# Optimization experiments

Measured on AMD Instinct MI355X. Metric: run time of the kernel, lower is better.

The kernel has to match this reference:

```python
import jax, jax.numpy as jnp
import numpy as np

B, N, D, H, SEEDS = 32, 2048, 256, 8, 32
DH = D // H
SCALE = 1.0 / np.sqrt(D)  # 1/sqrt(dim_V), as in MAB


def setup_inputs() -> dict:
    key = jax.random.key(0)
    ks = jax.random.split(key, 7)
    w_std = 1.0 / np.sqrt(D)  # ~ xavier scale for (D, D)
    x = jax.random.normal(ks[0], (B, N, D), dtype=jnp.float32)
    lengths = jax.random.randint(ks[1], (B,), 1, N + 1).astype(jnp.int64)
    S = jax.random.normal(ks[2], (1, SEEDS, D), dtype=jnp.float32) * w_std
    Wq = jax.random.normal(ks[3], (D, D), dtype=jnp.float32) * w_std
    Wk = jax.random.normal(ks[4], (D, D), dtype=jnp.float32) * w_std
    Wv = jax.random.normal(ks[5], (D, D), dtype=jnp.float32) * w_std
    Wo = jax.random.normal(ks[6], (D, D), dtype=jnp.float32) * w_std
    return {"x": x, "lengths": lengths, "S": S, "Wq": Wq, "Wk": Wk, "Wv": Wv, "Wo": Wo}


def reference(x, lengths, S, Wq, Wk, Wv, Wo):
    # PMA with norm=None: seeds attend over the (length-masked) input set.
    b, n, d = x.shape
    seeds = S.shape[1]
    # Linear projections (torch Linear: y = x @ W.T, bias=False)
    Q = jnp.einsum("bsd,ed->bse", jnp.broadcast_to(S, (b, seeds, d)), Wq)  # (B,SEEDS,D)
    K = jnp.einsum("bnd,ed->bne", x, Wk)  # (B,N,D)
    V = jnp.einsum("bnd,ed->bne", x, Wv)
    # mask=['K'] -> zero K,V rows beyond lengths
    col_mask = (jnp.arange(n)[None, :] < lengths[:, None]).astype(x.dtype)  # (B,N)
    K = K * col_mask[:, :, None]
    V = V * col_mask[:, :, None]
    # head split: (h b) s d  <=>  b h s d
    Qh = Q.reshape(b, seeds, H, DH).transpose(0, 2, 1, 3)  # (B,H,SEEDS,DH)
    Kh = K.reshape(b, n, H, DH).transpose(0, 2, 1, 3)      # (B,H,N,DH)
    Vh = V.reshape(b, n, H, DH).transpose(0, 2, 1, 3)
    scores = jnp.einsum("bhsd,bhnd->bhsn", Qh, Kh) * SCALE  # (B,H,SEEDS,N)
    exp = jnp.exp(scores)
    # set_softmax: two-sided length masks, normalize over keys with +1e-15
    row_mask = (jnp.arange(seeds)[None, :] < lengths[:, None]).astype(x.dtype)  # (B,SEEDS)
    exp = exp * row_mask[:, None, :, None] * col_mask[:, None, None, :]
    A = exp / (exp.sum(axis=3, keepdims=True) + 1e-15)
    Oh = Qh + jnp.einsum("bhsn,bhnd->bhsd", A, Vh)  # residual on Q_
    O = Oh.transpose(0, 2, 1, 3).reshape(b, seeds, d)  # merge heads
    # norm0/norm1 are None (norm=None in PMA)
    O = O + jax.nn.relu(jnp.einsum("bse,de->bsd", O, Wo))
    O = O * row_mask[:, :, None]  # final apply_masks(O, lengths)
    lengths_out = jnp.minimum(jnp.full_like(lengths, seeds), lengths)
    return O, lengths_out
```

## Files before the change

kernel.cpp:

```cpp
#include <hip/hip_runtime.h>
#include <hip/hip_bf16.h>
#include <cstdint>

#define BATCH 32
#define NKEY 2048
#define DIM 256
#define NHEAD 8
#define SEEDS 32
#define DHEAD 32
#define SCALE 0.0625f
#define NCHUNK 16
#define KCH 128
#define KT 32
#define PART_BYTES 17408

typedef unsigned short u16;
typedef __attribute__((ext_vector_type(8))) short s16x8;
typedef __attribute__((ext_vector_type(8))) unsigned short u16x8;
typedef __attribute__((ext_vector_type(4))) unsigned short u16x4;
typedef __attribute__((ext_vector_type(4))) float f32x4;

__device__ __forceinline__ u16 f2bf(float f) {
    unsigned u = __float_as_uint(f);
    u += 0x7FFFu + ((u >> 16) & 1u);
    return (u16)(u >> 16);
}
__device__ __forceinline__ float bf2f(u16 h) {
    return __uint_as_float(((unsigned)h) << 16);
}
__device__ __forceinline__ int get_len(const int* lens, int b) {
    return (lens[1] == 0) ? lens[2 * b] : lens[b];
}
__device__ __forceinline__ u16x8 cvt8(const float* p) {
    f32x4 a = *(const f32x4*)p;
    f32x4 b = *(const f32x4*)(p + 4);
    u16x8 r;
    r[0] = f2bf(a[0]); r[1] = f2bf(a[1]); r[2] = f2bf(a[2]); r[3] = f2bf(a[3]);
    r[4] = f2bf(b[0]); r[5] = f2bf(b[1]); r[6] = f2bf(b[2]); r[7] = f2bf(b[3]);
    return r;
}
__device__ __forceinline__ void glds16(const u16* g, u16* l) {
    __builtin_amdgcn_global_load_lds(
        (const __attribute__((address_space(1))) unsigned int*)g,
        (__attribute__((address_space(3))) unsigned int*)l, 16, 0, 0);
}

#define XGROUPS 2097152
#define WGROUPS 16384
__global__ __launch_bounds__(256) void cvt_kernel(const float* __restrict__ x,
                                                  const float* __restrict__ Wk,
                                                  const float* __restrict__ Wv,
                                                  u16* __restrict__ xb,
                                                  u16* __restrict__ wb) {
    size_t g = (size_t)blockIdx.x * 256 + threadIdx.x;
    size_t stride = (size_t)gridDim.x * 256;
    for (; g < XGROUPS + WGROUPS; g += stride) {
        const float* src;
        u16* dst;
        if (g < XGROUPS) {
            src = x + g * 8;
            dst = xb + g * 8;
        } else {
            size_t gw = g - XGROUPS;
            dst = wb + gw * 8;
            src = (gw < 8192) ? (Wk + gw * 8) : (Wv + (gw - 8192) * 8);
        }
        *(u16x8*)dst = cvt8(src);
    }
}

__global__ __launch_bounds__(256) void qproj_kernel(const float* __restrict__ S,
                                                    const float* __restrict__ Wq,
                                                    float* __restrict__ qf) {
    int s = blockIdx.x;
    int e = threadIdx.x;
    __shared__ float srow[DIM];
    srow[e] = S[s * DIM + e];
    __syncthreads();
    const float* wr = Wq + (size_t)e * DIM;
    float acc = 0.f;
#pragma unroll 4
    for (int d = 0; d < DIM; d += 4) {
        f32x4 w = *(const f32x4*)(wr + d);
        acc += srow[d] * w[0] + srow[d + 1] * w[1] + srow[d + 2] * w[2] + srow[d + 3] * w[3];
    }
    qf[s * DIM + e] = acc;
}

#define BM 128
#define BN 128
#define BK 32

__global__ __launch_bounds__(256) void kv_gemm_kernel(const u16* __restrict__ xb,
                                                      const u16* __restrict__ wb,
                                                      u16* __restrict__ kg,
                                                      u16* __restrict__ vt) {
    __shared__ u16 Alds[BM * BK];
    __shared__ u16 Blds[BM * BK];
    int bid = blockIdx.x;
    int swz = (bid & 7) * 256 + (bid >> 3);
    int nb = swz & 3;
    int mb = swz >> 2;
    const u16* asrc = xb + (size_t)mb * BM * DIM;
    const u16* bsrc = wb + (size_t)nb * BN * DIM;

    int tid = threadIdx.x;
    int lane = tid & 63;
    int wid = tid >> 6;
    int wr = wid >> 1, wc = wid & 1;
    int k8 = (lane >> 4) * 8;
    int fr = lane & 15;

    int srow = wid * 32 + (lane >> 2);
    int scol = (lane & 3) * 8;

    f32x4 acc[4][4];
#pragma unroll
    for (int m = 0; m < 4; m++)
#pragma unroll
        for (int n = 0; n < 4; n++) acc[m][n] = (f32x4){0.f, 0.f, 0.f, 0.f};

    for (int k0 = 0; k0 < DIM; k0 += BK) {
        const u16* ga = asrc + (size_t)srow * DIM + k0 + scol;
        const u16* gb = bsrc + (size_t)srow * DIM + k0 + scol;
        glds16(ga,            &Alds[(wid * 32) * BK]);
        glds16(ga + 16 * DIM, &Alds[(wid * 32 + 16) * BK]);
        glds16(gb,            &Blds[(wid * 32) * BK]);
        glds16(gb + 16 * DIM, &Blds[(wid * 32 + 16) * BK]);
        __syncthreads();

        s16x8 af[4], bfg[4];
#pragma unroll
        for (int m = 0; m < 4; m++)
            af[m] = *(const s16x8*)&Alds[(wr * 64 + m * 16 + fr) * BK + k8];
#pragma unroll
        for (int n = 0; n < 4; n++)
            bfg[n] = *(const s16x8*)&Blds[(wc * 64 + n * 16 + fr) * BK + k8];
#pragma unroll
        for (int m = 0; m < 4; m++)
#pragma unroll
            for (int n = 0; n < 4; n++)
                acc[m][n] = __builtin_amdgcn_mfma_f32_16x16x32_bf16(af[m], bfg[n], acc[m][n], 0, 0, 0);
        __syncthreads();
    }

    int gmbase = mb * BM + wr * 64 + (lane >> 4) * 4;
    int gnbase = nb * BN + wc * 64 + fr;
#pragma unroll
    for (int m = 0; m < 4; m++) {
        int r0 = gmbase + m * 16;
#pragma unroll
        for (int n = 0; n < 4; n++) {
            int gc = gnbase + n * 16;
            if (gc < 256) {
#pragma unroll
                for (int q = 0; q < 4; q++) {
                    int r = r0 + q;
                    kg[(size_t)r * 256 + (gc ^ ((r & 7) << 3))] = f2bf(acc[m][n][q]);
                }
            } else {
                int dh = gc - 256;
                int bidx = r0 >> 11, key = r0 & 2047;
                u16x4 v = {f2bf(acc[m][n][0]), f2bf(acc[m][n][1]),
                           f2bf(acc[m][n][2]), f2bf(acc[m][n][3])};
                *(u16x4*)&vt[((size_t)bidx * 256 + dh) * NKEY + key] = v;
            }
        }
    }
}

__global__ __launch_bounds__(512) void attn_kernel(const u16* __restrict__ kg,
                                                   const u16* __restrict__ vt,
                                                   const float* __restrict__ qf,
                                                   const int* __restrict__ lens,
                                                   char* __restrict__ partials) {
    int b = blockIdx.y, chunk = blockIdx.x;
    int len = get_len(lens, b);
    int n0 = chunk * KCH;
    int n1 = min(n0 + KCH, len);
    int tid = threadIdx.x;
    int lane = tid & 63;
    int h = tid >> 6;
    int fr = lane & 15;
    int g = lane >> 4;
    int k8 = g * 8;

    __shared__ u16 Klds[KT * 256];
    __shared__ u16 VTlds[256 * KT];
    __shared__ u16 Plds[NHEAD][32][32];

    s16x8 qb[2];
    qb[0] = (s16x8)cvt8(qf + (size_t)(fr) * DIM + h * DHEAD + k8);
    qb[1] = (s16x8)cvt8(qf + (size_t)(16 + fr) * DIM + h * DHEAD + k8);

    f32x4 accp[2][2];
#pragma unroll
    for (int i = 0; i < 2; i++)
#pragma unroll
        for (int j = 0; j < 2; j++) accp[i][j] = (f32x4){0.f, 0.f, 0.f, 0.f};
    float dsum[2] = {0.f, 0.f};

    int nk = n1 - n0;
    int nsteps = (nk > 0) ? ((nk + KT - 1) / KT) : 0;

    for (int t = 0; t < nsteps; t++) {
        {
            const u16* gk = kg + ((size_t)(b * NKEY + n0 + t * KT + h * 4) + (lane >> 5)) * 256
                               + (lane & 31) * 8;
            glds16(gk,           &Klds[(h * 4) * 256]);
            glds16(gk + 2 * 256, &Klds[(h * 4 + 2) * 256]);
            const u16* gv = vt + ((size_t)b * 256 + h * 32 + (lane >> 2)) * NKEY
                               + (n0 + t * KT) + (lane & 3) * 8;
            glds16(gv,            &VTlds[(h * 32) * KT]);
            glds16(gv + 16 * NKEY, &VTlds[(h * 32 + 16) * KT]);
        }
        __syncthreads();

        int rem = nk - t * KT;

        s16x8 ka[2];
#pragma unroll
        for (int m = 0; m < 2; m++)
            ka[m] = *(const s16x8*)&Klds[(m * 16 + fr) * 256 + (((h * 4 + g) ^ (fr & 7)) << 3)];
        f32x4 sc[2][2];
#pragma unroll
        for (int m = 0; m < 2; m++)
#pragma unroll
            for (int n = 0; n < 2; n++) {
                f32x4 z = (f32x4){0.f, 0.f, 0.f, 0.f};
                sc[m][n] = __builtin_amdgcn_mfma_f32_16x16x32_bf16(ka[m], qb[n], z, 0, 0, 0);
            }

#pragma unroll
        for (int m = 0; m < 2; m++) {
            int kbase = m * 16 + g * 4;
            int col = (((kbase >> 3) ^ (fr & 3)) << 3) + (kbase & 7);
#pragma unroll
            for (int n = 0; n < 2; n++) {
                u16x4 pv;
#pragma unroll
                for (int q = 0; q < 4; q++) {
                    float e = (kbase + q < rem) ? __expf(sc[m][n][q] * SCALE) : 0.f;
                    dsum[n] += e;
                    pv[q] = f2bf(e);
                }
                *(u16x4*)&Plds[h][n * 16 + fr][col] = pv;
            }
        }

        s16x8 pa[2], vb[2];
        int rcol = (g ^ (fr & 3)) << 3;
#pragma unroll
        for (int m = 0; m < 2; m++)
            pa[m] = *(const s16x8*)&Plds[h][m * 16 + fr][rcol];
#pragma unroll
        for (int n = 0; n < 2; n++)
            vb[n] = *(const s16x8*)&VTlds[(h * 32 + n * 16 + fr) * KT + k8];
#pragma unroll
        for (int m = 0; m < 2; m++)
#pragma unroll
            for (int n = 0; n < 2; n++)
                accp[m][n] = __builtin_amdgcn_mfma_f32_16x16x32_bf16(pa[m], vb[n], accp[m][n], 0, 0, 0);
        __syncthreads();
    }

    dsum[0] += __shfl_xor(dsum[0], 16);
    dsum[0] += __shfl_xor(dsum[0], 32);
    dsum[1] += __shfl_xor(dsum[1], 16);
    dsum[1] += __shfl_xor(dsum[1], 32);

    char* pb = partials + ((size_t)b * NCHUNK + chunk) * PART_BYTES;
    u16* pnum = (u16*)pb;
    float* pden = (float*)(pb + 16384);
#pragma unroll
    for (int m = 0; m < 2; m++)
#pragma unroll
        for (int n = 0; n < 2; n++)
#pragma unroll
            for (int q = 0; q < 4; q++)
                pnum[(size_t)(m * 16 + g * 4 + q) * DIM + h * DHEAD + n * 16 + fr] =
                    f2bf(accp[m][n][q]);
    if (lane < 16) {
        pden[h * 32 + fr] = dsum[0];
        pden[h * 32 + 16 + fr] = dsum[1];
    }
}

__global__ __launch_bounds__(256) void reduce_kernel(const char* __restrict__ partials,
                                                     const float* __restrict__ qf,
                                                     const int* __restrict__ lens,
                                                     float* __restrict__ opre,
                                                     float* __restrict__ outlen) {
    int b = blockIdx.x;
    int p = threadIdx.x;
    int h = p >> 5, s = p & 31;
    float denom = 0.f;
    float num[DHEAD];
#pragma unroll
    for (int j = 0; j < DHEAD; j++) num[j] = 0.f;
    for (int c = 0; c < NCHUNK; c++) {
        const char* pb = partials + ((size_t)b * NCHUNK + c) * PART_BYTES;
        denom += ((const float*)(pb + 16384))[p];
        const u16* pn = (const u16*)pb;
#pragma unroll
        for (int j = 0; j < DHEAD; j += 8) {
            u16x8 u = *(const u16x8*)&pn[(size_t)s * DIM + h * DHEAD + j];
#pragma unroll
            for (int t = 0; t < 8; t++) num[j + t] += bf2f(u[t]);
        }
    }
    float inv = 1.f / (denom + 1e-15f);
    size_t obase = ((size_t)b * SEEDS + s) * DIM + h * DHEAD;
#pragma unroll
    for (int j = 0; j < DHEAD; j++) {
        opre[obase + j] = qf[s * DIM + h * DHEAD + j] + num[j] * inv;
    }
    if (p == 0) outlen[b] = (float)min(SEEDS, get_len(lens, b));
}

__global__ __launch_bounds__(256) void epilogue_kernel(const float* __restrict__ opre,
                                                       const float* __restrict__ Wo,
                                                       const int* __restrict__ lens,
                                                       float* __restrict__ out) {
    int s = blockIdx.x, b = blockIdx.y;
    int d = threadIdx.x;
    size_t rbase = ((size_t)b * SEEDS + s) * DIM;
    if (s >= get_len(lens, b)) {
        out[rbase + d] = 0.f;
        return;
    }
    __shared__ float orow[DIM];
    orow[d] = opre[rbase + d];
    __syncthreads();
    const float* wrow = Wo + (size_t)d * DIM;
    float acc = 0.f;
#pragma unroll 4
    for (int e = 0; e < DIM; e += 4) {
        f32x4 w = *(const f32x4*)(wrow + e);
        acc += orow[e] * w[0] + orow[e + 1] * w[1] + orow[e + 2] * w[2] + orow[e + 3] * w[3];
    }
    out[rbase + d] = orow[d] + fmaxf(acc, 0.f);
}

extern "C" void kernel_launch(void* const* d_in, const int* in_sizes, int n_in,
                              void* d_out, int out_size, void* d_ws, size_t ws_size,
                              hipStream_t stream) {
    const float* x  = (const float*)d_in[0];
    const int* lens = (const int*)d_in[1];
    const float* S  = (const float*)d_in[2];
    const float* Wq = (const float*)d_in[3];
    const float* Wk = (const float*)d_in[4];
    const float* Wv = (const float*)d_in[5];
    const float* Wo = (const float*)d_in[6];
    float* out = (float*)d_out;

    char* ws = (char*)d_ws;
    float* qf       = (float*)ws;
    float* opre     = (float*)(ws + 0x8000);
    u16*   wb       = (u16*)  (ws + 0x108000);
    u16*   xb       = (u16*)  (ws + 0x148000);
    char*  partials = (char*) (ws + 0x148000);
    u16*   kg       = (u16*)  (ws + 0x2148000);
    u16*   vt       = (u16*)  (ws + 0x4148000);

    cvt_kernel<<<dim3(2048), 256, 0, stream>>>(x, Wk, Wv, xb, wb);
    qproj_kernel<<<dim3(SEEDS), 256, 0, stream>>>(S, Wq, qf);
    kv_gemm_kernel<<<dim3(2048), 256, 0, stream>>>(xb, wb, kg, vt);
    attn_kernel<<<dim3(NCHUNK, BATCH), 512, 0, stream>>>(kg, vt, qf, lens, partials);
    reduce_kernel<<<dim3(BATCH), 256, 0, stream>>>(partials, qf, lens, opre,
                                                   out + (size_t)BATCH * SEEDS * DIM);
    epilogue_kernel<<<dim3(SEEDS, BATCH), 256, 0, stream>>>(opre, Wo, lens, out);
}
```

Measured before the change: 211.2 us.

## Double-buffer LDS in KV GEMM and attention, fold Q projection into convert kernel

```diff
diff --git a/kernel.cpp b/kernel.cpp
--- a/kernel.cpp
+++ b/kernel.cpp
@@ -47,13 +47,33 @@
 
 #define XGROUPS 2097152
 #define WGROUPS 16384
+#define CVTBLK 2048
 __global__ __launch_bounds__(256) void cvt_kernel(const float* __restrict__ x,
                                                   const float* __restrict__ Wk,
                                                   const float* __restrict__ Wv,
+                                                  const float* __restrict__ S,
+                                                  const float* __restrict__ Wq,
                                                   u16* __restrict__ xb,
-                                                  u16* __restrict__ wb) {
+                                                  u16* __restrict__ wb,
+                                                  float* __restrict__ qf) {
+    if (blockIdx.x >= CVTBLK) {
+        int s = blockIdx.x - CVTBLK;
+        int e = threadIdx.x;
+        __shared__ float srow[DIM];
+        srow[e] = S[s * DIM + e];
+        __syncthreads();
+        const float* wr = Wq + (size_t)e * DIM;
+        float acc = 0.f;
+#pragma unroll 4
+        for (int d = 0; d < DIM; d += 4) {
+            f32x4 w = *(const f32x4*)(wr + d);
+            acc += srow[d] * w[0] + srow[d + 1] * w[1] + srow[d + 2] * w[2] + srow[d + 3] * w[3];
+        }
+        qf[s * DIM + e] = acc;
+        return;
+    }
     size_t g = (size_t)blockIdx.x * 256 + threadIdx.x;
-    size_t stride = (size_t)gridDim.x * 256;
+    const size_t stride = (size_t)CVTBLK * 256;
     for (; g < XGROUPS + WGROUPS; g += stride) {
         const float* src;
         u16* dst;
@@ -69,24 +89,6 @@
     }
 }
 
-__global__ __launch_bounds__(256) void qproj_kernel(const float* __restrict__ S,
-                                                    const float* __restrict__ Wq,
-                                                    float* __restrict__ qf) {
-    int s = blockIdx.x;
-    int e = threadIdx.x;
-    __shared__ float srow[DIM];
-    srow[e] = S[s * DIM + e];
-    __syncthreads();
-    const float* wr = Wq + (size_t)e * DIM;
-    float acc = 0.f;
-#pragma unroll 4
-    for (int d = 0; d < DIM; d += 4) {
-        f32x4 w = *(const f32x4*)(wr + d);
-        acc += srow[d] * w[0] + srow[d + 1] * w[1] + srow[d + 2] * w[2] + srow[d + 3] * w[3];
-    }
-    qf[s * DIM + e] = acc;
-}
-
 #define BM 128
 #define BN 128
 #define BK 32
@@ -95,8 +97,8 @@
                                                       const u16* __restrict__ wb,
                                                       u16* __restrict__ kg,
                                                       u16* __restrict__ vt) {
-    __shared__ u16 Alds[BM * BK];
-    __shared__ u16 Blds[BM * BK];
+    __shared__ u16 Alds[2][BM * BK];
+    __shared__ u16 Blds[2][BM * BK];
     int bid = blockIdx.x;
     int swz = (bid & 7) * 256 + (bid >> 3);
     int nb = swz & 3;
@@ -113,6 +115,8 @@
 
     int srow = wid * 32 + (lane >> 2);
     int scol = (lane & 3) * 8;
+    const u16* ga0 = asrc + (size_t)srow * DIM + scol;
+    const u16* gb0 = bsrc + (size_t)srow * DIM + scol;
 
     f32x4 acc[4][4];
 #pragma unroll
@@ -120,22 +124,29 @@
 #pragma unroll
         for (int n = 0; n < 4; n++) acc[m][n] = (f32x4){0.f, 0.f, 0.f, 0.f};
 
-    for (int k0 = 0; k0 < DIM; k0 += BK) {
-        const u16* ga = asrc + (size_t)srow * DIM + k0 + scol;
-        const u16* gb = bsrc + (size_t)srow * DIM + k0 + scol;
-        glds16(ga,            &Alds[(wid * 32) * BK]);
-        glds16(ga + 16 * DIM, &Alds[(wid * 32 + 16) * BK]);
-        glds16(gb,            &Blds[(wid * 32) * BK]);
-        glds16(gb + 16 * DIM, &Blds[(wid * 32 + 16) * BK]);
-        __syncthreads();
-
+    glds16(ga0,            &Alds[0][(wid * 32) * BK]);
+    glds16(ga0 + 16 * DIM, &Alds[0][(wid * 32 + 16) * BK]);
+    glds16(gb0,            &Blds[0][(wid * 32) * BK]);
+    glds16(gb0 + 16 * DIM, &Blds[0][(wid * 32 + 16) * BK]);
+    __syncthreads();
+
+    for (int t = 0; t < DIM / BK; t++) {
+        int cur = t & 1;
+        if (t + 1 < DIM / BK) {
+            const u16* ga = ga0 + (t + 1) * BK;
+            const u16* gb = gb0 + (t + 1) * BK;
+            glds16(ga,            &Alds[cur ^ 1][(wid * 32) * BK]);
+            glds16(ga + 16 * DIM, &Alds[cur ^ 1][(wid * 32 + 16) * BK]);
+            glds16(gb,            &Blds[cur ^ 1][(wid * 32) * BK]);
+            glds16(gb + 16 * DIM, &Blds[cur ^ 1][(wid * 32 + 16) * BK]);
+        }
         s16x8 af[4], bfg[4];
 #pragma unroll
         for (int m = 0; m < 4; m++)
-            af[m] = *(const s16x8*)&Alds[(wr * 64 + m * 16 + fr) * BK + k8];
+            af[m] = *(const s16x8*)&Alds[cur][(wr * 64 + m * 16 + fr) * BK + k8];
 #pragma unroll
         for (int n = 0; n < 4; n++)
-            bfg[n] = *(const s16x8*)&Blds[(wc * 64 + n * 16 + fr) * BK + k8];
+            bfg[n] = *(const s16x8*)&Blds[cur][(wc * 64 + n * 16 + fr) * BK + k8];
 #pragma unroll
         for (int m = 0; m < 4; m++)
 #pragma unroll
@@ -185,8 +196,8 @@
     int g = lane >> 4;
     int k8 = g * 8;
 
-    __shared__ u16 Klds[KT * 256];
-    __shared__ u16 VTlds[256 * KT];
+    __shared__ u16 Klds[2][KT * 256];
+    __shared__ u16 VTlds[2][256 * KT];
     __shared__ u16 Plds[NHEAD][32][32];
 
     s16x8 qb[2];
@@ -203,25 +214,34 @@
     int nk = n1 - n0;
     int nsteps = (nk > 0) ? ((nk + KT - 1) / KT) : 0;
 
+    const u16* gk0 = kg + ((size_t)(b * NKEY + n0 + h * 4) + (lane >> 5)) * 256 + (lane & 31) * 8;
+    const u16* gv0 = vt + ((size_t)b * 256 + h * 32 + (lane >> 2)) * NKEY + n0 + (lane & 3) * 8;
+
+    if (nsteps > 0) {
+        glds16(gk0,             &Klds[0][(h * 4) * 256]);
+        glds16(gk0 + 2 * 256,   &Klds[0][(h * 4 + 2) * 256]);
+        glds16(gv0,             &VTlds[0][(h * 32) * KT]);
+        glds16(gv0 + 16 * NKEY, &VTlds[0][(h * 32 + 16) * KT]);
+        __syncthreads();
+    }
+
     for (int t = 0; t < nsteps; t++) {
-        {
-            const u16* gk = kg + ((size_t)(b * NKEY + n0 + t * KT + h * 4) + (lane >> 5)) * 256
-                               + (lane & 31) * 8;
-            glds16(gk,           &Klds[(h * 4) * 256]);
-            glds16(gk + 2 * 256, &Klds[(h * 4 + 2) * 256]);
-            const u16* gv = vt + ((size_t)b * 256 + h * 32 + (lane >> 2)) * NKEY
-                               + (n0 + t * KT) + (lane & 3) * 8;
-            glds16(gv,            &VTlds[(h * 32) * KT]);
-            glds16(gv + 16 * NKEY, &VTlds[(h * 32 + 16) * KT]);
-        }
-        __syncthreads();
+        int cur = t & 1;
+        if (t + 1 < nsteps) {
+            const u16* gk = gk0 + (size_t)(t + 1) * KT * 256;
+            const u16* gv = gv0 + (t + 1) * KT;
+            glds16(gk,             &Klds[cur ^ 1][(h * 4) * 256]);
+            glds16(gk + 2 * 256,   &Klds[cur ^ 1][(h * 4 + 2) * 256]);
+            glds16(gv,             &VTlds[cur ^ 1][(h * 32) * KT]);
+            glds16(gv + 16 * NKEY, &VTlds[cur ^ 1][(h * 32 + 16) * KT]);
+        }
 
         int rem = nk - t * KT;
 
         s16x8 ka[2];
 #pragma unroll
         for (int m = 0; m < 2; m++)
-            ka[m] = *(const s16x8*)&Klds[(m * 16 + fr) * 256 + (((h * 4 + g) ^ (fr & 7)) << 3)];
+            ka[m] = *(const s16x8*)&Klds[cur][(m * 16 + fr) * 256 + (((h * 4 + g) ^ (fr & 7)) << 3)];
         f32x4 sc[2][2];
 #pragma unroll
         for (int m = 0; m < 2; m++)
@@ -255,7 +275,7 @@
             pa[m] = *(const s16x8*)&Plds[h][m * 16 + fr][rcol];
 #pragma unroll
         for (int n = 0; n < 2; n++)
-            vb[n] = *(const s16x8*)&VTlds[(h * 32 + n * 16 + fr) * KT + k8];
+            vb[n] = *(const s16x8*)&VTlds[cur][(h * 32 + n * 16 + fr) * KT + k8];
 #pragma unroll
         for (int m = 0; m < 2; m++)
 #pragma unroll
@@ -363,8 +383,7 @@
     u16*   kg       = (u16*)  (ws + 0x2148000);
     u16*   vt       = (u16*)  (ws + 0x4148000);
 
-    cvt_kernel<<<dim3(2048), 256, 0, stream>>>(x, Wk, Wv, xb, wb);
-    qproj_kernel<<<dim3(SEEDS), 256, 0, stream>>>(S, Wq, qf);
+    cvt_kernel<<<dim3(CVTBLK + SEEDS), 256, 0, stream>>>(x, Wk, Wv, S, Wq, xb, wb, qf);
     kv_gemm_kernel<<<dim3(2048), 256, 0, stream>>>(xb, wb, kg, vt);
     attn_kernel<<<dim3(NCHUNK, BATCH), 512, 0, stream>>>(kg, vt, qf, lens, partials);
     reduce_kernel<<<dim3(BATCH), 256, 0, stream>>>(partials, qf, lens, opre,
```

Result: no change. 207.3 us (-1.8%).
